# Kernel optimization log

Hardware: AMD Instinct MI355X
Metric: run time of the kernel (lower is better)

Reference implementation:

```python
import jax, jax.numpy as jnp
import numpy as np

V, BLK, L, H, E = 50257, 1024, 12, 12, 768
HS = E // H
B = 2


def _ln(x, w, b, eps=1e-5):
    mu = jnp.mean(x, axis=-1, keepdims=True)
    var = jnp.mean((x - mu) ** 2, axis=-1, keepdims=True)
    return (x - mu) * jax.lax.rsqrt(var + eps) * w + b


def setup_inputs() -> dict:
    key = jax.random.key(0)
    ks = jax.random.split(key, 16)
    s = 0.02
    inp = {
        "x": jax.random.randint(ks[0], (B, BLK), 0, V),
        "tok_emb": jax.random.normal(ks[1], (V, E), jnp.float32) * s,
        "pos_emb": jax.random.normal(ks[2], (BLK, E), jnp.float32) * s,
        "qW": jax.random.normal(ks[3], (L, H, HS, E), jnp.float32) * s,
        "kW": jax.random.normal(ks[4], (L, H, HS, E), jnp.float32) * s,
        "vW": jax.random.normal(ks[5], (L, H, HS, E), jnp.float32) * s,
        "ln1_w": jnp.ones((L, E), jnp.float32),
        "ln1_b": jnp.zeros((L, E), jnp.float32),
        "fc1_w": jax.random.normal(ks[6], (L, 4 * E, E), jnp.float32) * s,
        "fc1_b": jnp.zeros((L, 4 * E), jnp.float32),
        "fc2_w": jax.random.normal(ks[7], (L, E, 4 * E), jnp.float32) * s,
        "fc2_b": jnp.zeros((L, E), jnp.float32),
        "ln2_w": jnp.ones((L, E), jnp.float32),
        "ln2_b": jnp.zeros((L, E), jnp.float32),
        "lnf_w": jnp.ones((E,), jnp.float32),
        "lnf_b": jnp.zeros((E,), jnp.float32),
        "lm_w": jax.random.normal(ks[8], (V, E), jnp.float32) * s,
    }
    return inp


def _gpt(x, tok_emb, pos_emb, qW, kW, vW, ln1_w, ln1_b, fc1_w, fc1_b,
         fc2_w, fc2_b, ln2_w, ln2_b, lnf_w, lnf_b, lm_w):
    T = x.shape[1]
    h = tok_emb[x] + pos_emb[None, :T]  # [B,T,E]
    scale = 1.0 / jnp.sqrt(jnp.asarray(E, h.dtype))  # C**0.5 with C=n_embd
    causal = jnp.tril(jnp.ones((T, T), bool))  # mask where tril==0
    for l in range(L):
        q = jnp.einsum("bte,hde->bthd", h, qW[l])
        k = jnp.einsum("bte,hde->bthd", h, kW[l])
        v = jnp.einsum("bte,hde->bthd", h, vW[l])
        # faithful to source: w = k @ q^T / sqrt(n_embd); rows index k, cols index q
        w = jnp.einsum("bshd,bthd->bhst", k, q) * scale
        w = jnp.where(causal[None, None], w, -jnp.inf)
        w = jax.nn.softmax(w, axis=-1)
        a = jnp.einsum("bhst,bthd->bshd", w, v)  # [B,T,H,HS]
        a = a.reshape(a.shape[0], T, E)  # head-major concat
        h = _ln(h + a, ln1_w[l], ln1_b[l])
        m = jax.nn.gelu(jnp.einsum("bte,fe->btf", h, fc1_w[l]) + fc1_b[l],
                        approximate=False)
        m = jnp.einsum("btf,ef->bte", m, fc2_w[l]) + fc2_b[l]
        h = _ln(h + m, ln2_w[l], ln2_b[l])
    h = _ln(h, lnf_w, lnf_b)
    return jnp.einsum("bte,ve->btv", h, lm_w)


def reference(x, tok_emb, pos_emb, qW, kW, vW, ln1_w, ln1_b, fc1_w, fc1_b,
              fc2_w, fc2_b, ln2_w, ln2_b, lnf_w, lnf_b, lm_w):
    return _gpt(x, tok_emb, pos_emb, qW, kW, vW, ln1_w, ln1_b, fc1_w, fc1_b,
                fc2_w, fc2_b, ln2_w, ln2_b, lnf_w, lnf_b, lm_w)
```

## Files before the change

kernel.cpp:

```cpp
#include <hip/hip_runtime.h>
#include <math.h>

typedef unsigned short u16;
typedef __attribute__((ext_vector_type(8))) short short8;
typedef __attribute__((ext_vector_type(8))) u16 ushort8_t;
typedef __attribute__((ext_vector_type(4))) u16 ushort4_t;
typedef __attribute__((ext_vector_type(4))) float f32x4;

#define BB 2
#define TT 1024
#define EE 768
#define HH 12
#define HSZ 64
#define LL 12
#define FF 3072
#define VV 50257
#define VPAD 50304
#define MM 2048
#define NQKV 2304
#define QKW 1536
#define KVB 128
#define BK 64

__device__ __forceinline__ float bf2f(u16 u) {
    union { unsigned int i; float f; } c;
    c.i = ((unsigned int)u) << 16;
    return c.f;
}
__device__ __forceinline__ u16 f2bf(float f) {
    unsigned int u = __float_as_uint(f);
    unsigned int r = (u + 0x7FFFu + ((u >> 16) & 1u)) >> 16;
    return (u16)r;
}

__device__ __forceinline__ void gload_lds16(const void* g, void* l) {
    __builtin_amdgcn_global_load_lds(
        (const __attribute__((address_space(1))) unsigned int*)g,
        (__attribute__((address_space(3))) unsigned int*)l,
        16, 0, 0);
}

template<int N> __device__ __forceinline__ void waitcnt_vm() {
    if      constexpr (N == 0)  asm volatile("s_waitcnt vmcnt(0)" ::: "memory");
    else if constexpr (N == 4)  asm volatile("s_waitcnt vmcnt(4)" ::: "memory");
    else if constexpr (N == 6)  asm volatile("s_waitcnt vmcnt(6)" ::: "memory");
    else if constexpr (N == 8)  asm volatile("s_waitcnt vmcnt(8)" ::: "memory");
    else if constexpr (N == 12) asm volatile("s_waitcnt vmcnt(12)" ::: "memory");
    else static_assert(N == 0, "unsupported vmcnt");
}

__device__ __forceinline__ void xcd_swizzle(int& bx, int& by) {
    int nx = gridDim.x;
    int nwg = nx * gridDim.y;
    int orig = blockIdx.x + blockIdx.y * nx;
    int q = nwg >> 3, r = nwg & 7;
    int xcd = orig & 7, idx = orig >> 3;
    int nf = (xcd < r ? xcd * (q + 1) : r * (q + 1) + (xcd - r) * q) + idx;
    bx = nf % nx;
    by = nf / nx;
}

__global__ __launch_bounds__(256)
void cast_all_kernel(const float* __restrict__ qW, const float* __restrict__ kW,
                     const float* __restrict__ vW, const float* __restrict__ fc1w,
                     const float* __restrict__ fc2w, const float* __restrict__ lmw,
                     u16* __restrict__ wqkv, u16* __restrict__ wfc1,
                     u16* __restrict__ wfc2, u16* __restrict__ wlm)
{
    const int j = blockIdx.y;
    const float* s;
    u16* d;
    long total, per, stride;
    switch (j) {
    case 0: s = qW;   d = wqkv;              total = (long)LL * EE * EE; per = (long)EE * EE; stride = (long)NQKV * EE; break;
    case 1: s = kW;   d = wqkv + EE * EE;     total = (long)LL * EE * EE; per = (long)EE * EE; stride = (long)NQKV * EE; break;
    case 2: s = vW;   d = wqkv + 2 * EE * EE; total = (long)LL * EE * EE; per = (long)EE * EE; stride = (long)NQKV * EE; break;
    case 3: s = fc1w; d = wfc1;              total = (long)LL * FF * EE; per = total; stride = total; break;
    case 4: s = fc2w; d = wfc2;              total = (long)LL * EE * FF; per = total; stride = total; break;
    default: s = lmw; d = wlm;               total = (long)VV * EE;      per = total; stride = total; break;
    }
    long step = (long)gridDim.x * blockDim.x * 4;
    for (long i = ((long)blockIdx.x * blockDim.x + threadIdx.x) * 4; i < total; i += step) {
        long layer = i / per;
        long off = i - layer * per;
        float4 v = *reinterpret_cast<const float4*>(s + i);
        ushort4_t o;
        o[0] = f2bf(v.x); o[1] = f2bf(v.y); o[2] = f2bf(v.z); o[3] = f2bf(v.w);
        *reinterpret_cast<ushort4_t*>(d + layer * stride + off) = o;
    }
}

__global__ __launch_bounds__(256)
void embed_kernel(const int* __restrict__ x, const float* __restrict__ tok,
                  const float* __restrict__ pos, float* __restrict__ h,
                  u16* __restrict__ hb)
{
    int row = blockIdx.x;
    int t = row & (TT - 1);
    int id = x[row];
    int tid = threadIdx.x;
    if (tid >= EE / 4) return;
    int col = tid * 4;
    float4 tv = *reinterpret_cast<const float4*>(tok + (size_t)id * EE + col);
    float4 pv = *reinterpret_cast<const float4*>(pos + (size_t)t * EE + col);
    float4 v;
    v.x = tv.x + pv.x; v.y = tv.y + pv.y; v.z = tv.z + pv.z; v.w = tv.w + pv.w;
    *reinterpret_cast<float4*>(h + (size_t)row * EE + col) = v;
    ushort4_t o;
    o[0] = f2bf(v.x); o[1] = f2bf(v.y); o[2] = f2bf(v.z); o[3] = f2bf(v.w);
    *reinterpret_cast<ushort4_t*>(hb + (size_t)row * EE + col) = o;
}

__global__ __launch_bounds__(256)
void add_ln_kernel(const float* __restrict__ hin, const float* __restrict__ add,
                   const float* __restrict__ add2,
                   const float* __restrict__ w, const float* __restrict__ bias,
                   float* __restrict__ hout, u16* __restrict__ hbout)
{
    int lane = threadIdx.x & 63, wv = threadIdx.x >> 6;
    int row = blockIdx.x * 4 + wv;
    const float* hp = hin + (size_t)row * EE;
    float x[12];
    float s = 0.f;
#pragma unroll
    for (int c = 0; c < 3; ++c) {
        float4 hv = *reinterpret_cast<const float4*>(hp + c * 256 + lane * 4);
        if (add) {
            float4 av = *reinterpret_cast<const float4*>(add + (size_t)row * EE + c * 256 + lane * 4);
            hv.x += av.x; hv.y += av.y; hv.z += av.z; hv.w += av.w;
        }
        if (add2) {
            float4 av = *reinterpret_cast<const float4*>(add2 + (size_t)row * EE + c * 256 + lane * 4);
            hv.x += av.x; hv.y += av.y; hv.z += av.z; hv.w += av.w;
        }
        x[c * 4 + 0] = hv.x; x[c * 4 + 1] = hv.y; x[c * 4 + 2] = hv.z; x[c * 4 + 3] = hv.w;
        s += hv.x + hv.y + hv.z + hv.w;
    }
#pragma unroll
    for (int o = 32; o > 0; o >>= 1) s += __shfl_xor(s, o);
    float mu = s * (1.0f / EE);
    float vs = 0.f;
#pragma unroll
    for (int i = 0; i < 12; ++i) { float d = x[i] - mu; vs += d * d; }
#pragma unroll
    for (int o = 32; o > 0; o >>= 1) vs += __shfl_xor(vs, o);
    float inv = 1.0f / sqrtf(vs * (1.0f / EE) + 1e-5f);
#pragma unroll
    for (int c = 0; c < 3; ++c) {
        int col = c * 256 + lane * 4;
        float4 wv4 = *reinterpret_cast<const float4*>(w + col);
        float4 bv4 = *reinterpret_cast<const float4*>(bias + col);
        float4 o;
        o.x = (x[c * 4 + 0] - mu) * inv * wv4.x + bv4.x;
        o.y = (x[c * 4 + 1] - mu) * inv * wv4.y + bv4.y;
        o.z = (x[c * 4 + 2] - mu) * inv * wv4.z + bv4.z;
        o.w = (x[c * 4 + 3] - mu) * inv * wv4.w + bv4.w;
        *reinterpret_cast<float4*>(hout + (size_t)row * EE + col) = o;
        ushort4_t ob;
        ob[0] = f2bf(o.x); ob[1] = f2bf(o.y); ob[2] = f2bf(o.z); ob[3] = f2bf(o.w);
        *reinterpret_cast<ushort4_t*>(hbout + (size_t)row * EE + col) = ob;
    }
}

enum { EPI_GELU_BF16 = 1, EPI_BIAS_F32 = 2, EPI_F32 = 3, EPI_QKV = 4 };

template<int EPI, bool NGUARD, int DEPTH, int WM, int WN, int MR, int NR, bool KSPLIT = false>
__global__ __launch_bounds__(WM * WN * 64, 2)
void gemm_kernel(const u16* __restrict__ A, const u16* __restrict__ Bw,
                 const float* __restrict__ bias, void* __restrict__ Cout,
                 void* __restrict__ vTout, int Ndim, int Kdim, int Kstride)
{
    constexpr int NW  = WM * WN;
    constexpr int BMT = WM * MR * 16;
    constexpr int BNT = WN * NR * 16;
    constexpr int CA  = BMT / (8 * NW);
    constexpr int CB  = BNT / (8 * NW);
    constexpr int NLD = CA + CB;
    static_assert(BMT % (8 * NW) == 0 && BNT % (8 * NW) == 0, "stage geom");
    __shared__ u16 As[DEPTH * BMT * BK];
    __shared__ u16 Bs[DEPTH * BNT * BK];
    const int tid = threadIdx.x;
    const int lane = tid & 63;
    const int wid = tid >> 6;
    const int wm = wid / WN, wn = wid % WN;
    int bx, by;
    xcd_swizzle(bx, by);
    const int rowBase = bx * BMT;
    const int colBase = by * BNT;

    const u16* Ab = A + (KSPLIT ? (size_t)blockIdx.z * Kdim : 0);
    const u16* Bb = Bw + (KSPLIT ? (size_t)blockIdx.z * Kdim : 0);

    const int srow = lane >> 3;
    const int scol = ((lane & 7) ^ srow) * 8;

#define GSTAGE(k0_, buf_)                                                          \
    {                                                                              \
        _Pragma("unroll")                                                          \
        for (int i_ = 0; i_ < CA; ++i_) {                                          \
            int r0_ = (wid * CA + i_) * 8;                                         \
            gload_lds16(Ab + (size_t)(rowBase + r0_ + srow) * Kstride + (k0_) + scol, \
                        As + (buf_) * (BMT * BK) + r0_ * BK);                      \
        }                                                                          \
        _Pragma("unroll")                                                          \
        for (int i_ = 0; i_ < CB; ++i_) {                                          \
            int r0_ = (wid * CB + i_) * 8;                                         \
            gload_lds16(Bb + (size_t)(colBase + r0_ + srow) * Kstride + (k0_) + scol, \
                        Bs + (buf_) * (BNT * BK) + r0_ * BK);                      \
        }                                                                          \
    }

#define COMPUTE(Asb_, Bsb_)                                                       \
    {                                                                             \
        const int fr = lane & 15;                                                 \
        const int qd = lane >> 4;                                                 \
        _Pragma("unroll")                                                         \
        for (int kk = 0; kk < 2; ++kk) {                                          \
            short8 af[MR], bfr[NR];                                               \
            int goff = (((kk * 4 + qd) ^ (fr & 7))) * 8;                          \
            _Pragma("unroll")                                                     \
            for (int mi = 0; mi < MR; ++mi)                                       \
                af[mi] = *reinterpret_cast<const short8*>(                        \
                    &(Asb_)[(wm * (MR * 16) + mi * 16 + fr) * BK + goff]);        \
            _Pragma("unroll")                                                     \
            for (int ni = 0; ni < NR; ++ni)                                       \
                bfr[ni] = *reinterpret_cast<const short8*>(                       \
                    &(Bsb_)[(wn * (NR * 16) + ni * 16 + fr) * BK + goff]);        \
            _Pragma("unroll")                                                     \
            for (int mi = 0; mi < MR; ++mi)                                       \
                _Pragma("unroll")                                                 \
                for (int ni = 0; ni < NR; ++ni)                                   \
                    acc[mi][ni] = __builtin_amdgcn_mfma_f32_16x16x32_bf16(        \
                        af[mi], bfr[ni], acc[mi][ni], 0, 0, 0);                   \
        }                                                                         \
    }

    f32x4 acc[MR][NR] = {};
    const int nk = Kdim / BK;

    if (DEPTH > 1) {
#pragma unroll
        for (int p = 0; p < DEPTH; ++p) GSTAGE(p * BK, p)
        int cur = 0;
        for (int t = 0; t < nk; ++t) {
            int rem = nk - 1 - t;
            if (rem >= DEPTH - 1)            waitcnt_vm<NLD * (DEPTH - 1)>();
            else if (DEPTH > 2 && rem == 1)  waitcnt_vm<NLD>();
            else                             waitcnt_vm<0>();
            __builtin_amdgcn_s_barrier();
            const u16* Asb = As + cur * (BMT * BK);
            const u16* Bsb = Bs + cur * (BNT * BK);
            COMPUTE(Asb, Bsb)
            __builtin_amdgcn_s_barrier();
            if (t + DEPTH < nk) GSTAGE((t + DEPTH) * BK, cur)
            cur = (cur + 1 == DEPTH) ? 0 : cur + 1;
        }
    } else {
        for (int t = 0; t < nk; ++t) {
            GSTAGE(t * BK, 0)
            __syncthreads();
            COMPUTE(As, Bs)
            __syncthreads();
        }
    }

    if (EPI == EPI_QKV && colBase >= QKW) {
        u16* T = Bs;
        __syncthreads();
#pragma unroll
        for (int mi = 0; mi < MR; ++mi)
#pragma unroll
            for (int ni = 0; ni < NR; ++ni)
#pragma unroll
                for (int r = 0; r < 4; ++r) {
                    int lr = wm * (MR * 16) + mi * 16 + (lane >> 4) * 4 + r;
                    int lc = wn * (NR * 16) + ni * 16 + (lane & 15);
                    T[lc * 72 + lr] = f2bf(acc[mi][ni][r]);
                }
        __syncthreads();
        constexpr int SEGS = BMT / 32;
        int hdl = tid / SEGS;
        int seg = (tid % SEGS) * 32;
        if (hdl < BNT) {
            int b_ = rowBase >> 10;
            int t0 = rowBase & (TT - 1);
            u16* dst = (u16*)vTout + ((size_t)b_ * EE + (colBase - QKW) + hdl) * TT + t0 + seg;
            const u16* src = T + hdl * 72 + seg;
#pragma unroll
            for (int j = 0; j < 4; ++j)
                *reinterpret_cast<ushort8_t*>(dst + j * 8) =
                    *reinterpret_cast<const ushort8_t*>(src + j * 8);
        }
        return;
    }

    const size_t zoff = KSPLIT ? (size_t)blockIdx.z * MM * Ndim : 0;
#pragma unroll
    for (int mi = 0; mi < MR; ++mi) {
#pragma unroll
        for (int ni = 0; ni < NR; ++ni) {
#pragma unroll
            for (int r = 0; r < 4; ++r) {
                int row = rowBase + wm * (MR * 16) + mi * 16 + (lane >> 4) * 4 + r;
                int col = colBase + wn * (NR * 16) + ni * 16 + (lane & 15);
                if (NGUARD && col >= Ndim) continue;
                float v = acc[mi][ni][r];
                if (EPI == EPI_GELU_BF16) { v += bias[col]; v = 0.5f * v * (1.0f + erff(v * 0.70710678f)); }
                if (EPI == EPI_BIAS_F32)  { if (!KSPLIT || blockIdx.z == 0) v += bias[col]; }
                size_t idx = (size_t)row * Ndim + col;
                if (EPI == EPI_QKV) {
                    ((u16*)Cout)[(size_t)row * QKW + col] = f2bf(v);
                } else if (EPI == EPI_GELU_BF16) {
                    ((u16*)Cout)[idx] = f2bf(v);
                } else {
                    ((float*)Cout)[zoff + idx] = v;
                }
            }
        }
    }
}

__global__ __launch_bounds__(256)
void attn_kernel(const u16* __restrict__ qkb, const u16* __restrict__ vT,
                 float* __restrict__ aout)
{
    __shared__ u16 Qs[2 * KVB * 64];
    __shared__ u16 Vs[2 * 64 * KVB];
    __shared__ u16 Ps[4 * 16 * KVB];

    const int lane = threadIdx.x & 63;
    const int wv = threadIdx.x >> 6;
    int bxs, bys;
    xcd_swizzle(bxs, bys);
    const int js = (gridDim.x - 1) - bxs;
    const int s0 = js * 64;
    const int smax = s0 + 63;
    const int bh = bys;
    const int b = bh / HH, h = bh % HH;
    const int bT = b * TT;
    const float scale = 0.036084392f;

    short8 af[2];
    {
        int srow = bT + s0 + wv * 16 + (lane & 15);
#pragma unroll
        for (int kk = 0; kk < 2; ++kk)
            af[kk] = *reinterpret_cast<const short8*>(
                qkb + (size_t)srow * QKW + EE + h * HSZ + kk * 32 + (lane >> 4) * 8);
    }

    const int ntiles = (s0 + 63) / KVB + 1;
    const int qrow = lane >> 3;
    const int qu = lane & 7;
    const int vrow = lane >> 4;
    const int vu = lane & 15;

#define ASTAGE(jt2_, buf_)                                                            \
    {                                                                                 \
        int tb_ = (jt2_) * KVB;                                                       \
        _Pragma("unroll")                                                             \
        for (int i_ = 0; i_ < 4; ++i_) {                                              \
            int R0_ = wv * 32 + i_ * 8;                                               \
            int row_ = R0_ + qrow;                                                    \
            gload_lds16(qkb + (size_t)(bT + tb_ + row_) * QKW + h * HSZ               \
                            + ((qu ^ (row_ & 7)) * 8),                                \
                        &Qs[(buf_) * (KVB * 64) + R0_ * 64]);                         \
        }                                                                             \
        _Pragma("unroll")                                                             \
        for (int i_ = 0; i_ < 4; ++i_) {                                              \
            int R0_ = wv * 16 + i_ * 4;                                               \
            int row_ = R0_ + vrow;                                                    \
            gload_lds16(vT + ((size_t)b * EE + h * HSZ + row_) * TT + tb_             \
                            + ((vu ^ (row_ & 15)) * 8),                               \
                        &Vs[(buf_) * (64 * KVB) + R0_ * KVB]);                        \
        }                                                                             \
    }

    ASTAGE(0, 0)

    float m[4], l[4];
    f32x4 oacc[4] = {};
#pragma unroll
    for (int r = 0; r < 4; ++r) { m[r] = -INFINITY; l[r] = 0.f; }

    int cur = 0;
    for (int jt2 = 0; jt2 < ntiles; ++jt2) {
        __syncthreads();
        if (jt2 + 1 < ntiles) ASTAGE(jt2 + 1, cur ^ 1)

        const u16* Qb = &Qs[cur * (KVB * 64)];
        const u16* Vb = &Vs[cur * (64 * KVB)];
        const int tb = jt2 * KVB;
        const int navail = smax - tb;
        const int nact = min(8, (navail >> 4) + 1);
        const int nkc  = min(4, (navail >> 5) + 1);
        const bool dg = (tb + KVB - 1 > s0);

        f32x4 sc[8];
#pragma unroll
        for (int ni = 0; ni < 8; ++ni) {
            if (ni < nact) {
                f32x4 a = {};
                int trow = ni * 16 + (lane & 15);
#pragma unroll
                for (int kk = 0; kk < 2; ++kk) {
                    int g = kk * 4 + (lane >> 4);
                    short8 bq = *reinterpret_cast<const short8*>(
                        &Qb[trow * 64 + ((g ^ (trow & 7)) * 8)]);
                    a = __builtin_amdgcn_mfma_f32_16x16x32_bf16(af[kk], bq, a, 0, 0, 0);
                }
                sc[ni] = a;
            } else {
                f32x4 mn = {-1e30f, -1e30f, -1e30f, -1e30f};
                sc[ni] = mn;
            }
        }

        if (dg) {
#pragma unroll
            for (int ni = 0; ni < 8; ++ni)
#pragma unroll
                for (int r = 0; r < 4; ++r) {
                    float sv = sc[ni][r] * scale;
                    int t = tb + ni * 16 + (lane & 15);
                    int s = s0 + wv * 16 + (lane >> 4) * 4 + r;
                    if (t > s) sv = -1e30f;
                    sc[ni][r] = sv;
                }
        } else {
#pragma unroll
            for (int ni = 0; ni < 8; ++ni)
#pragma unroll
                for (int r = 0; r < 4; ++r) sc[ni][r] *= scale;
        }

        f32x4 pexp[8];
#pragma unroll
        for (int r = 0; r < 4; ++r) {
            float rm = sc[0][r];
#pragma unroll
            for (int ni = 1; ni < 8; ++ni) rm = fmaxf(rm, sc[ni][r]);
#pragma unroll
            for (int o = 1; o < 16; o <<= 1) rm = fmaxf(rm, __shfl_xor(rm, o));
            float mnew = fmaxf(m[r], rm);
            float alpha = __expf(m[r] - mnew);
            m[r] = mnew;
            float rs = 0.f;
#pragma unroll
            for (int ni = 0; ni < 8; ++ni) {
                float p;
                if (ni < nact) p = __expf(sc[ni][r] - mnew);
                else p = 0.f;
                pexp[ni][r] = p;
                rs += p;
            }
#pragma unroll
            for (int o = 1; o < 16; o <<= 1) rs += __shfl_xor(rs, o);
            l[r] = l[r] * alpha + rs;
#pragma unroll
            for (int dt = 0; dt < 4; ++dt) oacc[dt][r] *= alpha;
        }

        const int nst = nkc * 2;
#pragma unroll
        for (int ni = 0; ni < 8; ++ni) {
            if (ni < nst) {
#pragma unroll
                for (int r = 0; r < 4; ++r) {
                    int sl = (lane >> 4) * 4 + r;
                    int tl = ni * 16 + (lane & 15);
                    Ps[wv * (16 * KVB) + sl * KVB + (((tl >> 3) ^ sl) & 15) * 8 + (tl & 7)]
                        = f2bf(pexp[ni][r]);
                }
            }
        }

#pragma unroll
        for (int kc = 0; kc < 4; ++kc) {
            if (kc < nkc) {
                int srow = lane & 15;
                int g = kc * 4 + (lane >> 4);
                short8 pa = *reinterpret_cast<const short8*>(
                    &Ps[wv * (16 * KVB) + srow * KVB + ((g ^ srow) & 15) * 8]);
#pragma unroll
                for (int dt = 0; dt < 4; ++dt) {
                    int drow = dt * 16 + (lane & 15);
                    short8 bv = *reinterpret_cast<const short8*>(
                        &Vb[drow * KVB + (((kc * 4 + (lane >> 4)) ^ drow) & 15) * 8]);
                    oacc[dt] = __builtin_amdgcn_mfma_f32_16x16x32_bf16(pa, bv, oacc[dt], 0, 0, 0);
                }
            }
        }
        cur ^= 1;
    }

    float invl[4];
#pragma unroll
    for (int r = 0; r < 4; ++r) invl[r] = 1.0f / l[r];
#pragma unroll
    for (int dt = 0; dt < 4; ++dt)
#pragma unroll
        for (int r = 0; r < 4; ++r) {
            int sg = s0 + wv * 16 + (lane >> 4) * 4 + r;
            aout[(size_t)(bT + sg) * EE + h * HSZ + dt * 16 + (lane & 15)] =
                oacc[dt][r] * invl[r];
        }
}

extern "C" void kernel_launch(void* const* d_in, const int* in_sizes, int n_in,
                              void* d_out, int out_size, void* d_ws, size_t ws_size,
                              hipStream_t stream)
{
    const int*   x    = (const int*)d_in[0];
    const float* tok  = (const float*)d_in[1];
    const float* pos  = (const float*)d_in[2];
    const float* qW   = (const float*)d_in[3];
    const float* kW   = (const float*)d_in[4];
    const float* vW   = (const float*)d_in[5];
    const float* ln1w = (const float*)d_in[6];
    const float* ln1b = (const float*)d_in[7];
    const float* fc1w = (const float*)d_in[8];
    const float* fc1b = (const float*)d_in[9];
    const float* fc2w = (const float*)d_in[10];
    const float* fc2b = (const float*)d_in[11];
    const float* ln2w = (const float*)d_in[12];
    const float* ln2b = (const float*)d_in[13];
    const float* lnfw = (const float*)d_in[14];
    const float* lnfb = (const float*)d_in[15];
    const float* lmw  = (const float*)d_in[16];
    float* out = (float*)d_out;

    char* ws = (char*)d_ws;
    u16* wqkv = (u16*)ws;  ws += (size_t)LL * NQKV * EE * 2;
    u16* wfc1 = (u16*)ws;  ws += (size_t)LL * FF * EE * 2;
    u16* wfc2 = (u16*)ws;  ws += (size_t)LL * EE * FF * 2;
    u16* wlm  = (u16*)ws;  ws += (size_t)VPAD * EE * 2;
    float* h    = (float*)ws; ws += (size_t)MM * EE * 4;
    float* tmp  = (float*)ws; ws += (size_t)2 * MM * EE * 4;
    float* tmp2 = tmp + (size_t)MM * EE;
    u16* qkb = (u16*)ws;      ws += (size_t)MM * QKW * 2;
    u16* vTb = (u16*)ws;      ws += (size_t)BB * EE * TT * 2;
    u16* hb  = (u16*)ws;      ws += (size_t)MM * EE * 2;
    u16* mb  = (u16*)ws;      ws += (size_t)MM * FF * 2;

    dim3 blk(256);

    cast_all_kernel<<<dim3(1024, 6), blk, 0, stream>>>(
        qW, kW, vW, fc1w, fc2w, lmw, wqkv, wfc1, wfc2, wlm);

    embed_kernel<<<MM, blk, 0, stream>>>(x, tok, pos, h, hb);

    dim3 gQKV(MM / 64, NQKV / 128);
    dim3 gF1(MM / 64, FF / 128);
    dim3 gF2(MM / 64, EE / 64, 2);
    dim3 gV(MM / 128, VPAD / 128);
    dim3 gAttn(TT / 64, BB * HH);

    for (int l = 0; l < LL; ++l) {
        gemm_kernel<EPI_QKV, false, 2, 2, 2, 2, 4><<<gQKV, blk, 0, stream>>>(
            hb, wqkv + (size_t)l * NQKV * EE, nullptr, qkb, vTb, NQKV, EE, EE);
        attn_kernel<<<gAttn, blk, 0, stream>>>(qkb, vTb, tmp);
        add_ln_kernel<<<MM / 4, blk, 0, stream>>>(h, tmp, nullptr,
                                                  ln1w + l * EE, ln1b + l * EE, h, hb);
        gemm_kernel<EPI_GELU_BF16, false, 2, 2, 2, 2, 4><<<gF1, blk, 0, stream>>>(
            hb, wfc1 + (size_t)l * FF * EE, fc1b + (size_t)l * FF, mb, nullptr, FF, EE, EE);
        gemm_kernel<EPI_BIAS_F32, false, 3, 2, 2, 2, 2, true><<<gF2, blk, 0, stream>>>(
            mb, wfc2 + (size_t)l * EE * FF, fc2b + (size_t)l * EE, tmp, nullptr,
            EE, FF / 2, FF);
        add_ln_kernel<<<MM / 4, blk, 0, stream>>>(h, tmp, tmp2,
                                                  ln2w + l * EE, ln2b + l * EE, h, hb);
    }
    add_ln_kernel<<<MM / 4, blk, 0, stream>>>(h, nullptr, nullptr, lnfw, lnfb, h, hb);
    gemm_kernel<EPI_F32, true, 1, 2, 2, 4, 4><<<gV, blk, 0, stream>>>(
        hb, wlm, nullptr, out, nullptr, VV, EE, EE);
}
```

Before: 1.732 ms.

## Read attention Q/V operands directly from global memory instead of LDS staging

```diff
diff --git a/kernel.cpp b/kernel.cpp
--- a/kernel.cpp
+++ b/kernel.cpp
@@ -324,8 +324,6 @@
 void attn_kernel(const u16* __restrict__ qkb, const u16* __restrict__ vT,
                  float* __restrict__ aout)
 {
-    __shared__ u16 Qs[2 * KVB * 64];
-    __shared__ u16 Vs[2 * 64 * KVB];
     __shared__ u16 Ps[4 * 16 * KVB];
 
     const int lane = threadIdx.x & 63;
@@ -350,46 +348,15 @@
     }
 
     const int ntiles = (s0 + 63) / KVB + 1;
-    const int qrow = lane >> 3;
-    const int qu = lane & 7;
-    const int vrow = lane >> 4;
-    const int vu = lane & 15;
-
-#define ASTAGE(jt2_, buf_)                                                            \
-    {                                                                                 \
-        int tb_ = (jt2_) * KVB;                                                       \
-        _Pragma("unroll")                                                             \
-        for (int i_ = 0; i_ < 4; ++i_) {                                              \
-            int R0_ = wv * 32 + i_ * 8;                                               \
-            int row_ = R0_ + qrow;                                                    \
-            gload_lds16(qkb + (size_t)(bT + tb_ + row_) * QKW + h * HSZ               \
-                            + ((qu ^ (row_ & 7)) * 8),                                \
-                        &Qs[(buf_) * (KVB * 64) + R0_ * 64]);                         \
-        }                                                                             \
-        _Pragma("unroll")                                                             \
-        for (int i_ = 0; i_ < 4; ++i_) {                                              \
-            int R0_ = wv * 16 + i_ * 4;                                               \
-            int row_ = R0_ + vrow;                                                    \
-            gload_lds16(vT + ((size_t)b * EE + h * HSZ + row_) * TT + tb_             \
-                            + ((vu ^ (row_ & 15)) * 8),                               \
-                        &Vs[(buf_) * (64 * KVB) + R0_ * KVB]);                        \
-        }                                                                             \
-    }
-
-    ASTAGE(0, 0)
+    const u16* qbase = qkb + (size_t)bT * QKW + h * HSZ;
+    const u16* vbase = vT + ((size_t)b * EE + h * HSZ) * TT;
 
     float m[4], l[4];
     f32x4 oacc[4] = {};
 #pragma unroll
     for (int r = 0; r < 4; ++r) { m[r] = -INFINITY; l[r] = 0.f; }
 
-    int cur = 0;
     for (int jt2 = 0; jt2 < ntiles; ++jt2) {
-        __syncthreads();
-        if (jt2 + 1 < ntiles) ASTAGE(jt2 + 1, cur ^ 1)
-
-        const u16* Qb = &Qs[cur * (KVB * 64)];
-        const u16* Vb = &Vs[cur * (64 * KVB)];
         const int tb = jt2 * KVB;
         const int navail = smax - tb;
         const int nact = min(8, (navail >> 4) + 1);
@@ -401,12 +368,11 @@
         for (int ni = 0; ni < 8; ++ni) {
             if (ni < nact) {
                 f32x4 a = {};
-                int trow = ni * 16 + (lane & 15);
+                int trow = tb + ni * 16 + (lane & 15);
 #pragma unroll
                 for (int kk = 0; kk < 2; ++kk) {
-                    int g = kk * 4 + (lane >> 4);
                     short8 bq = *reinterpret_cast<const short8*>(
-                        &Qb[trow * 64 + ((g ^ (trow & 7)) * 8)]);
+                        qbase + (size_t)trow * QKW + (kk * 4 + (lane >> 4)) * 8);
                     a = __builtin_amdgcn_mfma_f32_16x16x32_bf16(af[kk], bq, a, 0, 0, 0);
                 }
                 sc[ni] = a;
@@ -486,12 +452,11 @@
                 for (int dt = 0; dt < 4; ++dt) {
                     int drow = dt * 16 + (lane & 15);
                     short8 bv = *reinterpret_cast<const short8*>(
-                        &Vb[drow * KVB + (((kc * 4 + (lane >> 4)) ^ drow) & 15) * 8]);
+                        vbase + (size_t)drow * TT + tb + (kc * 4 + (lane >> 4)) * 8);
                     oacc[dt] = __builtin_amdgcn_mfma_f32_16x16x32_bf16(pa, bv, oacc[dt], 0, 0, 0);
                 }
             }
         }
-        cur ^= 1;
     }
 
     float invl[4];
```

After: 2.109 ms. 21.8% more time.
